# Kernel optimization log

Hardware: AMD Instinct MI355X
Metric: run time of the kernel (lower is better)

The kernel has to match this reference:

```python
import jax, jax.numpy as jnp
import numpy as np

# sarModule stage: in=256, out=512, blocks=2, stride=2, patch_groups=4, mask_size=7
B, C_IN, H, W = 32, 256, 56, 56
C_OUT = 512
PLANES = C_OUT // 4   # Bottleneck inner width = planes // expansion = 128
G = 4                 # patch_groups
MS = 7                # mask_size
TEMP = 1.0            # gumbel-softmax temperature


def conv(x, w, stride=1, pad=0, groups=1):
    return jax.lax.conv_general_dilated(
        x, w, (stride, stride), [(pad, pad), (pad, pad)],
        feature_group_count=groups,
        dimension_numbers=('NCHW', 'OIHW', 'NCHW'))


def bn(x, g, b):
    # BatchNorm in inference form with running_mean=0, running_var=1 folded in
    return x * g[None, :, None, None] + b[None, :, None, None]


def avgpool3s2(x):
    # nn.AvgPool2d(3, stride=2, padding=1), count_include_pad=True
    s = jax.lax.reduce_window(x, 0.0, jax.lax.add, (1, 1, 3, 3), (1, 1, 2, 2),
                              [(0, 0), (0, 0), (1, 1), (1, 1)])
    return s / 9.0


def setup_inputs() -> dict:
    key = jax.random.key(0)
    ks = iter(jax.random.split(key, 64))

    def w(shape):
        fan_in = int(np.prod(shape[1:]))
        return jax.random.normal(next(ks), shape, jnp.float32) * np.float32((2.0 / fan_in) ** 0.5)

    ones = lambda n: jnp.ones((n,), jnp.float32)
    zeros = lambda n: jnp.zeros((n,), jnp.float32)

    x = jax.random.normal(next(ks), (B, C_IN, H, W), jnp.float32)
    u = jax.random.uniform(next(ks), (B, 2, G, MS, MS), jnp.float32, 1e-6, 1.0 - 1e-6)
    gumbel_noise = -jnp.log(-jnp.log(u))

    return dict(
        x=x, gumbel_noise=gumbel_noise,
        # base Bottleneck (256->512, stride 2, downsample = avgpool + 1x1 conv + bn)
        b_w1=w((PLANES, C_IN, 1, 1)), b_g1=ones(PLANES), b_b1=zeros(PLANES),
        b_w2=w((PLANES, PLANES, 3, 3)), b_g2=ones(PLANES), b_b2=zeros(PLANES),
        b_w3=w((C_OUT, PLANES, 1, 1)), b_g3=ones(C_OUT), b_b3=zeros(C_OUT),
        b_dw=w((C_OUT, C_IN, 1, 1)), b_dg=ones(C_OUT), b_db=zeros(C_OUT),
        # refine Bottleneck (256->512, stride 1, downsample = 1x1 conv + bn)
        r_w1=w((PLANES, C_IN, 1, 1)), r_g1=ones(PLANES), r_b1=zeros(PLANES),
        r_w2=w((PLANES, PLANES, 3, 3)), r_g2=ones(PLANES), r_b2=zeros(PLANES),
        r_w3=w((C_OUT, PLANES, 1, 1)), r_g3=ones(C_OUT), r_b3=zeros(C_OUT),
        r_dw=w((C_OUT, C_IN, 1, 1)), r_dg=ones(C_OUT), r_db=zeros(C_OUT),
        # maskGen: grouped 3x3 conv (512 -> 4*G), bn, pool, grouped 1x1 fc (4*G -> 2*G)
        m_w=w((4 * G, C_OUT // G, 3, 3)), m_g=ones(4 * G), m_b=zeros(4 * G),
        m_fcw=w((2 * G, 4, 1, 1)),
        m_fcb=jnp.concatenate([0.1 * ones(G), 5.0 * ones(G)]),  # bias init from maskGen
        # fusion Bottleneck (512->512, stride 2, downsample = avgpool only)
        f_w1=w((PLANES, C_OUT, 1, 1)), f_g1=ones(PLANES), f_b1=zeros(PLANES),
        f_w2=w((PLANES, PLANES, 3, 3)), f_g2=ones(PLANES), f_b2=zeros(PLANES),
        f_w3=w((C_OUT, PLANES, 1, 1)), f_g3=ones(C_OUT), f_b3=zeros(C_OUT),
    )


def reference(x, gumbel_noise,
              b_w1, b_g1, b_b1, b_w2, b_g2, b_b2, b_w3, b_g3, b_b3, b_dw, b_dg, b_db,
              r_w1, r_g1, r_b1, r_w2, r_g2, r_b2, r_w3, r_g3, r_b3, r_dw, r_dg, r_db,
              m_w, m_g, m_b, m_fcw, m_fcb,
              f_w1, f_g1, f_b1, f_w2, f_g2, f_b2, f_w3, f_g3, f_b3):
    # ---- base branch: Bottleneck stride 2, last_relu=False -> [B,512,28,28]
    o = jax.nn.relu(bn(conv(x, b_w1), b_g1, b_b1))
    o = jax.nn.relu(bn(conv(o, b_w2, stride=2, pad=1), b_g2, b_b2))
    o = bn(conv(o, b_w3), b_g3, b_b3)
    x_base = o + bn(conv(avgpool3s2(x), b_dw), b_dg, b_db)

    # ---- maskGen on x_base
    gmap = jax.nn.relu(bn(conv(x_base, m_w, pad=1, groups=G), m_g, m_b))      # [B,16,28,28]
    hb = x_base.shape[2] // MS                                                 # adaptive avgpool 28->7
    gmap = gmap.reshape(B, 4 * G, MS, hb, MS, hb).mean(axis=(3, 5))            # [B,16,7,7]
    logits = conv(gmap, m_fcw, groups=G) + m_fcb[None, :, None, None]          # [B,8,7,7]
    logits = logits.reshape(B, 2, G, MS, MS)                                   # view(B,2,groups,ms,ms)
    # hard gumbel-softmax over dim 1 with straight-through estimator
    y = jax.nn.softmax((logits + gumbel_noise) / TEMP, axis=1)
    hard = jax.nn.one_hot(jnp.argmax(y, axis=1), 2, axis=1, dtype=y.dtype)
    gates = hard + y - jax.lax.stop_gradient(y)
    mask = gates[:, 1]                                                         # [B,G,7,7]

    # nearest-upsample mask x8 and expand across each channel group
    mask_up = jnp.repeat(jnp.repeat(mask, H // MS, axis=-2), W // MS, axis=-1) # [B,G,56,56]
    mask_full = jnp.broadcast_to(mask_up[:, :, None], (B, G, C_OUT // G, H, W)).reshape(B, C_OUT, H, W)

    # ---- refine branch: Bottleneck stride 1, output gated by mask, last_relu=False
    o = jax.nn.relu(bn(conv(x, r_w1), r_g1, r_b1))
    o = jax.nn.relu(bn(conv(o, r_w2, pad=1), r_g2, r_b2))
    o = bn(conv(o, r_w3), r_g3, r_b3) * mask_full
    x_refine = o + bn(conv(x, r_dw), r_dg, r_db)                               # [B,512,56,56]

    # ---- fuse: bilinear upsample base to refine resolution (align_corners=False)
    x_base_up = jax.image.resize(x_base, (B, C_OUT, H, W), 'bilinear')
    fused = jax.nn.relu(x_base_up + x_refine)

    # ---- fusion Bottleneck: stride 2, downsample = avgpool only, last_relu=True
    o = jax.nn.relu(bn(conv(fused, f_w1), f_g1, f_b1))
    o = jax.nn.relu(bn(conv(o, f_w2, stride=2, pad=1), f_g2, f_b2))
    o = bn(conv(o, f_w3), f_g3, f_b3)
    out = jax.nn.relu(o + avgpool3s2(fused))                                   # [B,512,28,28]
    return out, mask
```

## Files before the change

### kernel.cpp

```cpp
#include <hip/hip_runtime.h>
#include <cstdint>

#define BB   32
#define CINX 256
#define HH   56
#define WW   56
#define HWX  3136
#define CO   512
#define PL   128
#define HP   28
#define WP   28
#define HWP  784
#define NG   4
#define MSZ  7

typedef unsigned short ushortT;
typedef unsigned int   uint32;
typedef __attribute__((ext_vector_type(8))) short short8;
typedef __attribute__((ext_vector_type(4))) float f32x4;

__device__ __forceinline__ ushortT f2bf(float f){
  uint32 u = __float_as_uint(f);
  u = (u + 0x7fffu + ((u >> 16) & 1u)) >> 16;
  return (ushortT)u;
}
__device__ __forceinline__ float bf2f(ushortT u){
  return __uint_as_float(((uint32)u) << 16);
}
__device__ __forceinline__ void split2(float v, ushortT& h, ushortT& lo){
  h = f2bf(v);
  lo = f2bf(v - bf2f(h));
}
__device__ __forceinline__ uint32 packu(ushortT a, ushortT b){
  return (uint32)a | ((uint32)b << 16);
}

typedef __attribute__((address_space(1))) const void g_void;
typedef __attribute__((address_space(3))) void l_void;
__device__ __forceinline__ void glds16(const ushortT* g, ushortT* l){
  __builtin_amdgcn_global_load_lds((g_void*)g, (l_void*)l, 16, 0, 0);
}
__device__ __forceinline__ void waitcnt_vm8(){ asm volatile("s_waitcnt vmcnt(8)" ::: "memory"); }
__device__ __forceinline__ void waitcnt_vm0(){ asm volatile("s_waitcnt vmcnt(0)" ::: "memory"); }

__device__ __forceinline__ void wsplit(float v, ushortT* dh, ushortT* dl, size_t i){
  ushortT h, lo; split2(v, h, lo); dh[i] = h; dl[i] = lo;
}

__global__ __launch_bounds__(256) void prep_w(
  const float* __restrict__ b_w1, const float* __restrict__ b_g1,
  const float* __restrict__ b_w2, const float* __restrict__ b_g2,
  const float* __restrict__ b_w3, const float* __restrict__ b_g3,
  const float* __restrict__ b_dw, const float* __restrict__ b_dg,
  const float* __restrict__ r_w1, const float* __restrict__ r_g1,
  const float* __restrict__ r_w2, const float* __restrict__ r_g2,
  const float* __restrict__ r_w3, const float* __restrict__ r_g3,
  const float* __restrict__ r_dw, const float* __restrict__ r_dg,
  const float* __restrict__ f_w1, const float* __restrict__ f_g1,
  const float* __restrict__ f_w2, const float* __restrict__ f_g2,
  const float* __restrict__ f_w3, const float* __restrict__ f_g3,
  const float* __restrict__ b_b1, const float* __restrict__ r_b1,
  ushortT* __restrict__ dh, ushortT* __restrict__ dl,
  ushortT* __restrict__ zp, float* __restrict__ biasC)
{
  const int idx = blockIdx.x*256 + threadIdx.x;
  switch (blockIdx.y){
    case 0: {
      if (idx >= 32768) return; int m = idx >> 8;
      wsplit(b_w1[idx]*b_g1[m], dh, dl, (size_t)0 + idx); } break;
    case 3: {
      if (idx >= 32768) return; int m = idx >> 8;
      wsplit(r_w1[idx]*r_g1[m], dh, dl, 32768 + (size_t)idx); } break;
    case 1: {
      if (idx >= 147456) return; int m = idx / 1152; int k = idx - m*1152;
      int tap = k >> 7, c = k & 127;
      wsplit(b_w2[((size_t)(m*128 + c))*9 + tap]*b_g2[m], dh, dl, 65536 + (size_t)idx); } break;
    case 2: {
      if (idx >= 196608) return; int m = idx / 384; int k = idx - m*384;
      float v = (k < 128) ? b_w3[m*128 + k]*b_g3[m] : b_dw[m*256 + (k-128)]*b_dg[m];
      wsplit(v, dh, dl, 212992 + (size_t)idx); } break;
    case 4: {
      if (idx >= 147456) return; int m = idx / 1152; int k = idx - m*1152;
      int tap = k >> 7, c = k & 127;
      wsplit(r_w2[((size_t)(m*128 + c))*9 + tap]*r_g2[m], dh, dl, 409600 + (size_t)idx); } break;
    case 5: {
      if (idx >= 196608) return; int m = idx / 384; int k = idx - m*384;
      float v = (k < 128) ? r_w3[m*128 + k]*r_g3[m] : r_dw[m*256 + (k-128)]*r_dg[m];
      wsplit(v, dh, dl, 557056 + (size_t)idx); } break;
    case 6: {
      if (idx >= 65536) return; int m = idx >> 9;
      wsplit(f_w1[idx]*f_g1[m], dh, dl, 753664 + (size_t)idx); } break;
    case 7: {
      if (idx >= 147456) return; int m = idx / 1152; int k = idx - m*1152;
      int tap = k >> 7, c = k & 127;
      wsplit(f_w2[((size_t)(m*128 + c))*9 + tap]*f_g2[m], dh, dl, 819200 + (size_t)idx); } break;
    case 8: {
      if (idx >= 65536) return; int m = idx >> 7;
      wsplit(f_w3[idx]*f_g3[m], dh, dl, 966656 + (size_t)idx); } break;
    case 9: {
      if (idx < 64) zp[idx] = 0;
      if (idx < 128) biasC[idx] = b_b1[idx];
      else if (idx < 256) biasC[idx] = r_b1[idx-128];
    } break;
  }
}

__global__ __launch_bounds__(256) void k_pool2(const float* __restrict__ x,
    ushortT* __restrict__ ph_, ushortT* __restrict__ pl_){
  __shared__ float s[16][17];
  const int p0 = blockIdx.x*16, c0 = blockIdx.y*16, bz = blockIdx.z;
  const int ci = threadIdx.x >> 4, pi = threadIdx.x & 15;
  {
    const int p = p0 + pi;
    const int oy = p / WP, ox = p - oy*WP;
    const float* src = x + ((size_t)bz*CINX + c0 + ci)*HWX;
    float sum = 0.f;
    #pragma unroll
    for (int dy=0; dy<3; dy++){
      int yy = 2*oy-1+dy;
      if ((unsigned)yy >= HH) continue;
      #pragma unroll
      for (int dx=0; dx<3; dx++){
        int xx = 2*ox-1+dx;
        if ((unsigned)xx >= WW) continue;
        sum += src[yy*WW + xx];
      }
    }
    s[ci][pi] = sum * (1.f/9.f);
  }
  __syncthreads();
  const int pr = threadIdx.x >> 4, cj = threadIdx.x & 15;
  float v = s[cj][pr];
  ushortT h, lo; split2(v, h, lo);
  size_t o = ((size_t)bz*HWP + p0 + pr)*CINX + c0 + cj;
  ph_[o] = h; pl_[o] = lo;
}

__global__ __launch_bounds__(256) void prep_x2(const float* __restrict__ x,
    ushortT* __restrict__ xh, ushortT* __restrict__ xl){
  __shared__ float s[16][17];
  const int p0 = blockIdx.x*16, c0 = blockIdx.y*16, bz = blockIdx.z;
  const int ci = threadIdx.x >> 4, pi = threadIdx.x & 15;
  s[ci][pi] = x[((size_t)bz*CINX + c0 + ci)*HWX + p0 + pi];
  __syncthreads();
  const int pr = threadIdx.x >> 4, cj = threadIdx.x & 15;
  float v = s[cj][pr];
  ushortT h, lo; split2(v, h, lo);
  size_t o = ((size_t)bz*HWX + p0 + pr)*CINX + c0 + cj;
  xh[o] = h; xl[o] = lo;
}

__global__ __launch_bounds__(256) void k_poolf(const ushortT* __restrict__ fzh,
    const ushortT* __restrict__ fzl, float* __restrict__ pf){
  const int p = blockIdx.x, bz = blockIdx.y;
  const int oy = p / WP, ox = p - oy*WP;
  const int c = threadIdx.x*2;
  float s0 = 0.f, s1 = 0.f;
  #pragma unroll
  for (int dy=0; dy<3; dy++){
    const int iy = 2*oy - 1 + dy;
    if ((unsigned)iy >= (unsigned)HH) continue;
    #pragma unroll
    for (int dx=0; dx<3; dx++){
      const int ix = 2*ox - 1 + dx;
      if ((unsigned)ix >= (unsigned)WW) continue;
      const size_t fi = ((size_t)bz*HWX + (size_t)(iy*WW + ix))*CO + c;
      uint32 hh = *(const uint32*)(fzh + fi);
      uint32 ll = *(const uint32*)(fzl + fi);
      s0 += bf2f((ushortT)(hh & 0xffff)) + bf2f((ushortT)(ll & 0xffff));
      s1 += bf2f((ushortT)(hh >> 16))    + bf2f((ushortT)(ll >> 16));
    }
  }
  const size_t o = ((size_t)bz*HWP + p)*CO + c;
  pf[o]   = s0 * (1.f/9.f);
  pf[o+1] = s1 * (1.f/9.f);
}

template<int KIND,int EPI,int S1F,int MT,int DBUF,int SWAP,int GX,int GY,int STRIDE,int PAD,
         int HIN,int WIN,int WOUT,int NOUT,int C1,int C2,int BSTR1,int MTOT,int KTOT>
__global__ __launch_bounds__(MT*2)
void gemm_bf3(const ushortT* __restrict__ wph, const ushortT* __restrict__ wpl,
              const ushortT* __restrict__ s1h, const ushortT* __restrict__ s1l,
              const ushortT* __restrict__ s2h, const ushortT* __restrict__ s2l,
              const float* __restrict__ xf32,
              const float* __restrict__ bias1, const float* __restrict__ bias2,
              const float* __restrict__ maskf, const float* __restrict__ xbase,
              const ushortT* __restrict__ zp,
              ushortT* __restrict__ oh, ushortT* __restrict__ ol,
              float* __restrict__ of32)
{
  constexpr int NW = MT/32;
  constexpr int BCALLS = 8/NW;
  constexpr bool GATHER1 = (KIND==0 && S1F==1);
  constexpr int BUFSZ = MT*64 + 8192;
  constexpr int T = GX*GY*BB;
  static_assert(T % 8 == 0, "grid not divisible by 8 XCDs");
  constexpr int QX = T/8;
  __shared__ ushortT smem[BUFSZ*(DBUF+1)];

  const int tid = threadIdx.x;
  const int lin = blockIdx.x;
  const int virt = (lin & 7)*QX + (lin >> 3);
  const int vx = virt % GX;
  const int vrest = virt / GX;
  const int vy = vrest % GY;
  const int bz = vrest / GY;
  const int nt = SWAP ? vy : vx;
  const int mt = SWAP ? vx : vy;
  const int l  = tid & 63, w = tid >> 6;
  const int wm = w >> 1, wn = w & 1;

  size_t a_src[2]; int a_dst[2];
  #pragma unroll
  for (int c=0;c<2;c++){
    int s = (w*2 + c)*64 + l;
    int row = s >> 2, slotm = s & 3;
    int logical = slotm ^ ((row >> 1) & 3);
    a_src[c] = (size_t)(mt*MT + row)*KTOT + logical*8;
    a_dst[c] = (w*2 + c)*512;
  }

  int b_dst[2]; size_t b_base1[2], b_base2[2]; int b_klane[2];
  int b_oy[2], b_ox[2]; bool b_ok[2]; float b_mv[2];
  #pragma unroll
  for (int c=0;c<BCALLS;c++){
    int s = (w*BCALLS + c)*64 + l;
    int row = s >> 2, slotm = s & 3;
    int logical = slotm ^ ((row >> 1) & 3);
    b_klane[c] = logical*8;
    b_dst[c] = (w*BCALLS + c)*512;
    int ngr = nt*128 + row;
    b_ok[c] = (ngr < NOUT);
    int oyv = ngr / WOUT, oxv = ngr - (ngr / WOUT)*WOUT;
    b_oy[c] = oyv; b_ox[c] = oxv;
    b_base1[c] = ((size_t)bz*NOUT + ngr)*BSTR1 + b_klane[c];
    b_base2[c] = ((size_t)bz*NOUT + ngr)*C2 + b_klane[c];
    b_mv[c] = 1.f;
    if (KIND == 3)
      b_mv[c] = b_ok[c] ? maskf[((size_t)(bz*NG + mt)*MSZ + (oyv>>3))*MSZ + (oxv>>3)] : 0.f;
  }

  const int sr = tid >> 1;
  const int hp = tid & 1;
  const int swz = (sr >> 1) & 3;
  const int lws0 = sr*32 + ((2*hp) ^ swz)*8;
  const int lws1 = sr*32 + ((2*hp + 1) ^ swz)*8;
  const int ng = nt*128 + sr;

  f32x4 acc[4][4];
  f32x4 zf = {0.f,0.f,0.f,0.f};
  #pragma unroll
  for (int i=0;i<4;i++)
    #pragma unroll
    for (int j=0;j<4;j++) acc[i][j] = zf;

  auto stagef = [&](int ks, ushortT* AHb, ushortT* ALb, ushortT* BHb, ushortT* BLb){
    const int k0 = ks*32;
    #pragma unroll
    for (int c=0;c<2;c++){
      glds16(wph + a_src[c] + k0, AHb + a_dst[c]);
      glds16(wpl + a_src[c] + k0, ALb + a_dst[c]);
    }
    if constexpr (GATHER1){
      if (tid < 256){
        uint4 b0 = make_uint4(0,0,0,0), b1v = b0, b2v = b0, b3v = b0;
        if (ng < NOUT){
          size_t fbase = ((size_t)bz*C1 + k0 + hp*16)*(size_t)NOUT + ng;
          ushortT h[16], lo[16];
          #pragma unroll
          for (int e=0;e<16;e++){ split2(xf32[fbase + (size_t)e*NOUT], h[e], lo[e]); }
          b0  = make_uint4(packu(h[0],h[1]),  packu(h[2],h[3]),  packu(h[4],h[5]),  packu(h[6],h[7]));
          b1v = make_uint4(packu(h[8],h[9]),  packu(h[10],h[11]),packu(h[12],h[13]),packu(h[14],h[15]));
          b2v = make_uint4(packu(lo[0],lo[1]),packu(lo[2],lo[3]),packu(lo[4],lo[5]),packu(lo[6],lo[7]));
          b3v = make_uint4(packu(lo[8],lo[9]),packu(lo[10],lo[11]),packu(lo[12],lo[13]),packu(lo[14],lo[15]));
        }
        *(uint4*)(BHb + lws0) = b0;  *(uint4*)(BHb + lws1) = b1v;
        *(uint4*)(BLb + lws0) = b2v; *(uint4*)(BLb + lws1) = b3v;
      }
    } else {
      #pragma unroll
      for (int c=0;c<BCALLS;c++){
        const ushortT *sh, *sl;
        if constexpr (KIND == 0){
          bool ok = b_ok[c];
          size_t off = b_base1[c] + k0;
          sh = ok ? s1h + off : zp;  sl = ok ? s1l + off : zp;
        } else if constexpr (KIND == 1){
          const int tap = k0 >> 7;
          const int cb  = (k0 & 127);
          const int dy = tap/3, dx = tap - 3*(tap/3);
          int iy = b_oy[c]*STRIDE + dy - PAD;
          int ix = b_ox[c]*STRIDE + dx - PAD;
          bool ok = b_ok[c] && (unsigned)iy < (unsigned)HIN && (unsigned)ix < (unsigned)WIN;
          size_t off = ((size_t)bz*(HIN*WIN) + (size_t)(iy*WIN + ix))*BSTR1 + cb + b_klane[c];
          sh = ok ? s1h + off : zp;  sl = ok ? s1l + off : zp;
        } else {
          if (k0 < C1){
            bool ok = b_ok[c] && (KIND != 3 || b_mv[c] != 0.f);
            size_t off = b_base1[c] + k0;
            sh = ok ? s1h + off : zp;  sl = ok ? s1l + off : zp;
          } else {
            bool ok = b_ok[c];
            size_t off = b_base2[c] + (k0 - C1);
            sh = ok ? s2h + off : zp;  sl = ok ? s2l + off : zp;
          }
        }
        glds16(sh, BHb + b_dst[c]);
        glds16(sl, BLb + b_dst[c]);
      }
    }
  };

  auto computef = [&](const ushortT* AHb, const ushortT* ALb,
                      const ushortT* BHb, const ushortT* BLb){
    short8 bh[4], bl[4];
    #pragma unroll
    for (int nf=0; nf<4; nf++){
      const int rr = wn*64 + nf*16 + (l & 15);
      const int ph = (l >> 4) ^ ((rr >> 1) & 3);
      bh[nf] = *(const short8*)(BHb + rr*32 + ph*8);
      bl[nf] = *(const short8*)(BLb + rr*32 + ph*8);
    }
    #pragma unroll
    for (int mf=0; mf<4; mf++){
      const int rr = wm*64 + mf*16 + (l & 15);
      const int ph = (l >> 4) ^ ((rr >> 1) & 3);
      short8 ah = *(const short8*)(AHb + rr*32 + ph*8);
      short8 al = *(const short8*)(ALb + rr*32 + ph*8);
      #pragma unroll
      for (int nf=0; nf<4; nf++)
        acc[mf][nf] = __builtin_amdgcn_mfma_f32_16x16x32_bf16(ah, bh[nf], acc[mf][nf], 0,0,0);
      #pragma unroll
      for (int nf=0; nf<4; nf++)
        acc[mf][nf] = __builtin_amdgcn_mfma_f32_16x16x32_bf16(ah, bl[nf], acc[mf][nf], 0,0,0);
      #pragma unroll
      for (int nf=0; nf<4; nf++)
        acc[mf][nf] = __builtin_amdgcn_mfma_f32_16x16x32_bf16(al, bh[nf], acc[mf][nf], 0,0,0);
    }
  };

  const int NK = KTOT / 32;
  if constexpr (DBUF == 0){
    ushortT* AH  = smem;
    ushortT* AL  = smem + MT*32;
    ushortT* BHs = smem + MT*64;
    ushortT* BLs = smem + MT*64 + 4096;
    for (int ks=0; ks<NK; ks++){
      stagef(ks, AH, AL, BHs, BLs);
      __syncthreads();
      computef(AH, AL, BHs, BLs);
      __syncthreads();
    }
  } else {
    stagef(0, smem, smem + MT*32, smem + MT*64, smem + MT*64 + 4096);
    waitcnt_vm0();
    __builtin_amdgcn_s_barrier();
    for (int ks=0; ks<NK; ks++){
      ushortT* cb = smem + (ks & 1)*BUFSZ;
      ushortT* nb = smem + ((ks & 1) ^ 1)*BUFSZ;
      if (ks + 1 < NK){
        stagef(ks + 1, nb, nb + MT*32, nb + MT*64, nb + MT*64 + 4096);
        waitcnt_vm8();
      } else {
        waitcnt_vm0();
      }
      __builtin_amdgcn_sched_barrier(0);
      __builtin_amdgcn_s_barrier();
      computef(cb, cb + MT*32, cb + MT*64, cb + MT*64 + 4096);
      __builtin_amdgcn_s_barrier();
    }
  }

  const int mb0 = mt*MT + wm*64;
  const int nb0 = nt*128 + wn*64;

  #pragma unroll
  for (int nf=0; nf<4; nf++){
    const int n = nb0 + nf*16 + (l & 15);
    if (n >= NOUT) continue;
    if constexpr (EPI == 0){
      const size_t ob = ((size_t)bz*NOUT + n)*MTOT;
      #pragma unroll
      for (int mf=0; mf<4; mf++){
        const int m0 = mb0 + mf*16 + (l>>4)*4;
        ushort4 hq, lq; ushortT h0, l0; float v;
        v = fmaxf(acc[mf][nf][0] + bias1[m0+0], 0.f); split2(v,h0,l0); hq.x=h0; lq.x=l0;
        v = fmaxf(acc[mf][nf][1] + bias1[m0+1], 0.f); split2(v,h0,l0); hq.y=h0; lq.y=l0;
        v = fmaxf(acc[mf][nf][2] + bias1[m0+2], 0.f); split2(v,h0,l0); hq.z=h0; lq.z=l0;
        v = fmaxf(acc[mf][nf][3] + bias1[m0+3], 0.f); split2(v,h0,l0); hq.w=h0; lq.w=l0;
        *(ushort4*)(oh + ob + m0) = hq;
        *(ushort4*)(ol + ob + m0) = lq;
      }
    } else if constexpr (EPI == 1){
      #pragma unroll
      for (int mf=0; mf<4; mf++){
        const int m0 = mb0 + mf*16 + (l>>4)*4;
        #pragma unroll
        for (int r=0;r<4;r++){
          const int m = m0 + r;
          of32[((size_t)bz*MTOT + m)*NOUT + n] = acc[mf][nf][r] + bias1[m] + bias2[m];
        }
      }
    } else if constexpr (EPI == 2){
      const int y = n / WOUT, x = n - (n / WOUT)*WOUT;
      const int grpw = (mt*MT + wm*64) >> 7;
      const float mvv = maskf[((size_t)(bz*NG + grpw)*MSZ + (y>>3))*MSZ + (x>>3)];
      const int iy = y >> 1, ix = x >> 1;
      int yA,yB,xA,xB; float wyA,wyB,wxA,wxB;
      if (y & 1){ yA=iy; wyA=0.75f; yB=(iy+1<HP)?iy+1:HP-1; wyB=0.25f; }
      else      { yA=(iy>0)?iy-1:0; wyA=0.25f; yB=iy; wyB=0.75f; }
      if (x & 1){ xA=ix; wxA=0.75f; xB=(ix+1<WP)?ix+1:WP-1; wxB=0.25f; }
      else      { xA=(ix>0)?ix-1:0; wxA=0.25f; xB=ix; wxB=0.75f; }
      const size_t ob = ((size_t)bz*NOUT + n)*MTOT;
      #pragma unroll
      for (int mf=0; mf<4; mf++){
        const int m0 = mb0 + mf*16 + (l>>4)*4;
        ushort4 hq, lq;
        #pragma unroll
        for (int r=0;r<4;r++){
          const int m = m0 + r;
          const float* xb = xbase + ((size_t)bz*MTOT + m)*HWP;
          float up = wyA*(wxA*xb[yA*WP+xA] + wxB*xb[yA*WP+xB])
                   + wyB*(wxA*xb[yB*WP+xA] + wxB*xb[yB*WP+xB]);
          float v = fmaxf(acc[mf][nf][r] + up + mvv*bias1[m] + bias2[m], 0.f);
          ushortT h0, l0; split2(v, h0, l0);
          if      (r==0){hq.x=h0;lq.x=l0;}
          else if (r==1){hq.y=h0;lq.y=l0;}
          else if (r==2){hq.z=h0;lq.z=l0;}
          else          {hq.w=h0;lq.w=l0;}
        }
        *(ushort4*)(oh + ob + m0) = hq;
        *(ushort4*)(ol + ob + m0) = lq;
      }
    } else {
      const float* pfrow = xbase + ((size_t)bz*NOUT + n)*MTOT;
      #pragma unroll
      for (int mf=0; mf<4; mf++){
        const int m0 = mb0 + mf*16 + (l>>4)*4;
        const float4 pv = *(const float4*)(pfrow + m0);
        of32[((size_t)bz*MTOT + m0+0)*NOUT + n] = fmaxf(acc[mf][nf][0] + bias1[m0+0] + pv.x, 0.f);
        of32[((size_t)bz*MTOT + m0+1)*NOUT + n] = fmaxf(acc[mf][nf][1] + bias1[m0+1] + pv.y, 0.f);
        of32[((size_t)bz*MTOT + m0+2)*NOUT + n] = fmaxf(acc[mf][nf][2] + bias1[m0+2] + pv.z, 0.f);
        of32[((size_t)bz*MTOT + m0+3)*NOUT + n] = fmaxf(acc[mf][nf][3] + bias1[m0+3] + pv.w, 0.f);
      }
    }
  }
}

#define GM_LDSW 9216
__global__ __launch_bounds__(256) void k_gmap2(const float* __restrict__ xbase,
    const float* __restrict__ mw, const float* __restrict__ mg, const float* __restrict__ mb,
    float* __restrict__ gmap){
  __shared__ float wsh[GM_LDSW];
  __shared__ float red[16][2][4][16];
  const int tile = blockIdx.x, b = blockIdx.y;
  const int tid = threadIdx.x;
  const int pl = tid & 15, cs = tid >> 4;
  const int p = tile*16 + pl;
  const int oy = p / WP, ox = p - oy*WP;
  int toff[9];
  #pragma unroll
  for (int tap=0; tap<9; tap++){
    int dy = tap/3, dx = tap - 3*dy;
    int yy = oy + dy - 1, xx = ox + dx - 1;
    toff[tap] = ((unsigned)yy < (unsigned)HP && (unsigned)xx < (unsigned)WP) ? (yy*WP + xx) : -1;
  }
  float acc[2][4] = {{0.f,0.f,0.f,0.f},{0.f,0.f,0.f,0.f}};
  for (int pass=0; pass<2; pass++){
    __syncthreads();
    for (int i = tid; i < GM_LDSW; i += 256){
      int ocl = i & 3, tap = (i >> 2) % 9, c_rel = i / 36;
      int cg = pass*256 + c_rel;
      int g = cg >> 7;
      int oc = g*4 + ocl;
      wsh[i] = mw[((size_t)(oc*128 + (cg & 127)))*9 + tap] * mg[oc];
    }
    __syncthreads();
    const float* xb = xbase + ((size_t)b*CO + pass*256 + cs*16)*HWP;
    for (int cl=0; cl<16; cl++){
      const float* xc = xb + (size_t)cl*HWP;
      const float* wr = &wsh[(cs*16 + cl)*36];
      #pragma unroll
      for (int tap=0; tap<9; tap++){
        if (toff[tap] < 0) continue;
        float v = xc[toff[tap]];
        f32x4 w4 = *(const f32x4*)(wr + tap*4);
        acc[pass][0] += v*w4[0];
        acc[pass][1] += v*w4[1];
        acc[pass][2] += v*w4[2];
        acc[pass][3] += v*w4[3];
      }
    }
  }
  #pragma unroll
  for (int pp=0; pp<2; pp++)
    #pragma unroll
    for (int o=0; o<4; o++)
      red[cs][pp][o][pl] = acc[pp][o];
  __syncthreads();
  const int oc = tid >> 4;
  const int g = oc >> 2, ocl = oc & 3, pg = g >> 1, cs0 = (g & 1)*8;
  float s = 0.f;
  #pragma unroll
  for (int t=0; t<8; t++) s += red[cs0 + t][pg][ocl][pl];
  s = fmaxf(s + mb[oc], 0.f);
  gmap[((size_t)b*16 + oc)*HWP + p] = s;
}

__global__ __launch_bounds__(256) void k_gpool(const float* __restrict__ gmap, float* __restrict__ gpool){
  int idx = blockIdx.x*256 + threadIdx.x;
  if (idx >= BB*16*49) return;
  int q = idx % 49; int t = idx / 49; int ch = t % 16; int b = t / 16;
  int my = q/7, mx = q%7;
  const float* src = gmap + ((size_t)b*16 + ch)*HWP;
  float s = 0.f;
  #pragma unroll
  for (int yb=0;yb<4;yb++)
    #pragma unroll
    for (int xb=0;xb<4;xb++)
      s += src[(my*4+yb)*WP + (mx*4+xb)];
  gpool[idx] = s * (1.f/16.f);
}

__global__ __launch_bounds__(256) void k_mask(const float* __restrict__ gpool, const float* __restrict__ fcw,
    const float* __restrict__ fcb, const float* __restrict__ gum,
    float* __restrict__ maskf, float* __restrict__ mout){
// ... 28 lines not shown
  const float* b_w2 = (const float*)d_in[5];
  const float* b_g2 = (const float*)d_in[6];
  const float* b_b2 = (const float*)d_in[7];
  const float* b_w3 = (const float*)d_in[8];
  const float* b_g3 = (const float*)d_in[9];
  const float* b_b3 = (const float*)d_in[10];
  const float* b_dw = (const float*)d_in[11];
  const float* b_dg = (const float*)d_in[12];
  const float* b_db = (const float*)d_in[13];
  const float* r_w1 = (const float*)d_in[14];
  const float* r_g1 = (const float*)d_in[15];
  const float* r_b1 = (const float*)d_in[16];
  const float* r_w2 = (const float*)d_in[17];
  const float* r_g2 = (const float*)d_in[18];
  const float* r_b2 = (const float*)d_in[19];
  const float* r_w3 = (const float*)d_in[20];
  const float* r_g3 = (const float*)d_in[21];
  const float* r_b3 = (const float*)d_in[22];
  const float* r_dw = (const float*)d_in[23];
  const float* r_dg = (const float*)d_in[24];
  const float* r_db = (const float*)d_in[25];
  const float* m_w  = (const float*)d_in[26];
  const float* m_g  = (const float*)d_in[27];
  const float* m_b  = (const float*)d_in[28];
  const float* m_fcw= (const float*)d_in[29];
  const float* m_fcb= (const float*)d_in[30];
  const float* f_w1 = (const float*)d_in[31];
  const float* f_g1 = (const float*)d_in[32];
  const float* f_b1 = (const float*)d_in[33];
  const float* f_w2 = (const float*)d_in[34];
  const float* f_g2 = (const float*)d_in[35];
  const float* f_b2 = (const float*)d_in[36];
  const float* f_w3 = (const float*)d_in[37];
  const float* f_g3 = (const float*)d_in[38];
  const float* f_b3 = (const float*)d_in[39];

  char* ws = (char*)d_ws;
  constexpr size_t O_WPH  = 0;
  constexpr size_t O_WPL  = 2064384;
  constexpr size_t O_CH   = 4128768;
  constexpr size_t O_DH   = 55508992;
  constexpr size_t O_DL   = 61931520;
  constexpr size_t O_EH   = 68354048;
  constexpr size_t O_EL   = 94044160;
  constexpr size_t O_PF   = O_EH;
  constexpr size_t O_XB   = 119734272;
  constexpr size_t O_GMAP = 171114496;
  constexpr size_t O_GPOOL= 172720128;
  constexpr size_t O_MASK = 172820480;
  constexpr size_t O_FH   = 172845568;
  constexpr size_t O_PH   = 172845568;
  constexpr size_t O_PL   = 185690624;
  constexpr size_t O_FL   = 275606016;
  constexpr size_t O_ZP   = 378366464;
  constexpr size_t O_BIASC= 378366592;

  ushortT* WPH = (ushortT*)(ws + O_WPH);
  ushortT* WPL = (ushortT*)(ws + O_WPL);
  ushortT* MGH = (ushortT*)(ws + O_CH);
  ushortT* XH  = (ushortT*)(ws + O_CH);
  ushortT* F1H = (ushortT*)(ws + O_CH);
  ushortT* F1L = (ushortT*)(ws + O_CH + 25690112);
  ushortT* DHp = (ushortT*)(ws + O_DH);
  ushortT* DLp = (ushortT*)(ws + O_DL);
  ushortT* EHp = (ushortT*)(ws + O_EH);
  ushortT* ELp = (ushortT*)(ws + O_EL);
  float*   PF  = (float*)(ws + O_PF);
  float*   XB  = (float*)(ws + O_XB);
  ushortT* PHp = (ushortT*)(ws + O_PH);
  ushortT* PLp = (ushortT*)(ws + O_PL);
  ushortT* FHp = (ushortT*)(ws + O_FH);
  ushortT* FLp = (ushortT*)(ws + O_FL);
  float*   GMAP = (float*)(ws + O_GMAP);
  float*   GPOOL= (float*)(ws + O_GPOOL);
  float*   MASKF= (float*)(ws + O_MASK);
  ushortT* ZP  = (ushortT*)(ws + O_ZP);
  float*   BIASC = (float*)(ws + O_BIASC);
  (void)ws_size;

  float* outp = (float*)d_out;
  float* mout = outp + (size_t)BB*CO*HWP;
  ushortT* dout_u = (ushortT*)d_out;

  dim3 blk(256), blk2(512);
  const ushortT* nu = nullptr; const float* nf_ = nullptr;
  ushortT* nuo = nullptr; float* nfo = nullptr;

  prep_w<<<dim3(768, 10), blk, 0, stream>>>(b_w1,b_g1,b_w2,b_g2,b_w3,b_g3,b_dw,b_dg,
      r_w1,r_g1,r_w2,r_g2,r_w3,r_g3,r_dw,r_dg,f_w1,f_g1,f_w2,f_g2,f_w3,f_g3,
      b_b1, r_b1, WPH, WPL, ZP, BIASC);
  k_pool2<<<dim3(49, 16, BB), blk, 0, stream>>>(x, PHp, PLp);

  gemm_bf3<0,0,1,256,0,0, 25,1, 1,0,56,56,56,3136, 256,0,256, 256,256><<<dim3(800), blk2, 0, stream>>>(
      WPH+0, WPL+0, nu, nu, nu, nu, x, BIASC, nf_, nf_, nf_, ZP, MGH, dout_u, nfo);
  gemm_bf3<1,0,0,128,1,0, 7,1, 2,1,56,56,28,784, 128,0,256, 128,1152><<<dim3(224), blk, 0, stream>>>(
      WPH+65536, WPL+65536, MGH, dout_u, nu, nu, nf_, b_b2, nf_, nf_, nf_, ZP, DHp, DLp, nfo);
  gemm_bf3<2,1,0,256,0,0, 7,2, 1,0,28,28,28,784, 128,256,128, 512,384><<<dim3(448), blk2, 0, stream>>>(
      WPH+212992, WPL+212992, DHp, DLp, PHp, PLp, nf_, b_b3, b_db, nf_, nf_, ZP, nuo, nuo, XB);

  k_gmap2<<<dim3(49, BB), blk, 0, stream>>>(XB, m_w, m_g, m_b, GMAP);
  k_gpool<<<dim3(98), blk, 0, stream>>>(GMAP, GPOOL);
  k_mask<<<dim3(25), blk, 0, stream>>>(GPOOL, m_fcw, m_fcb, gum, MASKF, mout);

  gemm_bf3<1,0,0,128,1,0, 25,1, 1,1,56,56,56,3136, 128,0,256, 128,1152><<<dim3(800), blk, 0, stream>>>(
      WPH+409600, WPL+409600, MGH+128, dout_u+128, nu, nu, nf_, r_b2, nf_, nf_, nf_, ZP, EHp, ELp, nfo);

  prep_x2<<<dim3(196, 16, BB), blk, 0, stream>>>(x, XH, dout_u);

  gemm_bf3<3,2,0,128,1,1, 4,25, 1,0,56,56,56,3136, 128,256,128, 512,384><<<dim3(3200), blk, 0, stream>>>(
      WPH+557056, WPL+557056, EHp, ELp, XH, dout_u, nf_, r_b3, r_db, MASKF, XB, ZP, FHp, FLp, nfo);

  k_poolf<<<dim3(HWP, BB), blk, 0, stream>>>(FHp, FLp, PF);

  gemm_bf3<0,0,0,128,1,0, 25,1, 1,0,56,56,56,3136, 512,0,512, 128,512><<<dim3(800), blk, 0, stream>>>(
      WPH+753664, WPL+753664, FHp, FLp, nu, nu, nf_, f_b1, nf_, nf_, nf_, ZP, F1H, F1L, nfo);
  gemm_bf3<1,0,0,128,1,0, 7,1, 2,1,56,56,28,784, 128,0,128, 128,1152><<<dim3(224), blk, 0, stream>>>(
      WPH+819200, WPL+819200, F1H, F1L, nu, nu, nf_, f_b2, nf_, nf_, nf_, ZP, DHp, DLp, nfo);
  gemm_bf3<0,3,0,256,0,0, 7,2, 1,0,28,28,28,784, 128,0,128, 512,128><<<dim3(448), blk2, 0, stream>>>(
      WPH+966656, WPL+966656, DHp, DLp, nu, nu, nf_, f_b3, nf_, nf_, PF, ZP, nuo, nuo, outp);
}
```

Measured before the change: 1.054 ms.

## Stage GEMM epilogue output through LDS for coalesced stores; vectorize avg-pool kernel

For the bf16-split output epilogues (EPI 0 and 2), the high and low halves of each tile are written to shared memory one after the other. Each thread then writes a contiguous 64-element row segment to global memory with 16-byte stores, replacing scattered 8-byte stores. The pool kernel now handles 8 channels per thread and 4 output pixels per block, using 16-byte loads and float4 stores. The change adds extra barriers, LDS round-trips and register pressure (the low halves are held across the first store phase), and may raise shared memory use for kernels without double buffering.

```diff
diff --git a/kernel.cpp b/kernel.cpp
--- a/kernel.cpp
+++ b/kernel.cpp
@@ -152,10 +152,13 @@
 
 __global__ __launch_bounds__(256) void k_poolf(const ushortT* __restrict__ fzh,
     const ushortT* __restrict__ fzl, float* __restrict__ pf){
-  const int p = blockIdx.x, bz = blockIdx.y;
+  const int pb = blockIdx.x, bz = blockIdx.y;
+  const int psub = threadIdx.x >> 6;
+  const int lane = threadIdx.x & 63;
+  const int p = pb*4 + psub;
   const int oy = p / WP, ox = p - oy*WP;
-  const int c = threadIdx.x*2;
-  float s0 = 0.f, s1 = 0.f;
+  const int c = lane*8;
+  float s[8] = {0.f,0.f,0.f,0.f,0.f,0.f,0.f,0.f};
   #pragma unroll
   for (int dy=0; dy<3; dy++){
     const int iy = 2*oy - 1 + dy;
@@ -165,15 +168,19 @@
       const int ix = 2*ox - 1 + dx;
       if ((unsigned)ix >= (unsigned)WW) continue;
       const size_t fi = ((size_t)bz*HWX + (size_t)(iy*WW + ix))*CO + c;
-      uint32 hh = *(const uint32*)(fzh + fi);
-      uint32 ll = *(const uint32*)(fzl + fi);
-      s0 += bf2f((ushortT)(hh & 0xffff)) + bf2f((ushortT)(ll & 0xffff));
-      s1 += bf2f((ushortT)(hh >> 16))    + bf2f((ushortT)(ll >> 16));
+      uint4 hh = *(const uint4*)(fzh + fi);
+      uint4 ll = *(const uint4*)(fzl + fi);
+      ushortT hv[8], lv[8];
+      *(uint4*)hv = hh; *(uint4*)lv = ll;
+      #pragma unroll
+      for (int j=0;j<8;j++) s[j] += bf2f(hv[j]) + bf2f(lv[j]);
     }
   }
   const size_t o = ((size_t)bz*HWP + p)*CO + c;
-  pf[o]   = s0 * (1.f/9.f);
-  pf[o+1] = s1 * (1.f/9.f);
+  float4 o0 = make_float4(s[0]*(1.f/9.f), s[1]*(1.f/9.f), s[2]*(1.f/9.f), s[3]*(1.f/9.f));
+  float4 o1 = make_float4(s[4]*(1.f/9.f), s[5]*(1.f/9.f), s[6]*(1.f/9.f), s[7]*(1.f/9.f));
+  *(float4*)(pf + o)     = o0;
+  *(float4*)(pf + o + 4) = o1;
 }
 
 template<int KIND,int EPI,int S1F,int MT,int DBUF,int SWAP,int GX,int GY,int STRIDE,int PAD,
@@ -193,10 +200,14 @@
   constexpr int BCALLS = 8/NW;
   constexpr bool GATHER1 = (KIND==0 && S1F==1);
   constexpr int BUFSZ = MT*64 + 8192;
+  constexpr int SSTR = MT + 8;
+  constexpr int STORE_USH = (EPI==0 || EPI==2) ? 128*SSTR : 0;
+  constexpr int STAGE_USH = BUFSZ*(DBUF+1);
+  constexpr int SMEM_USH = (STAGE_USH > STORE_USH) ? STAGE_USH : STORE_USH;
   constexpr int T = GX*GY*BB;
   static_assert(T % 8 == 0, "grid not divisible by 8 XCDs");
   constexpr int QX = T/8;
-  __shared__ ushortT smem[BUFSZ*(DBUF+1)];
+  __shared__ ushortT smem[SMEM_USH];
 
   const int tid = threadIdx.x;
   const int lin = blockIdx.x;
@@ -374,74 +385,122 @@
   const int mb0 = mt*MT + wm*64;
   const int nb0 = nt*128 + wn*64;
 
-  #pragma unroll
-  for (int nf=0; nf<4; nf++){
-    const int n = nb0 + nf*16 + (l & 15);
-    if (n >= NOUT) continue;
-    if constexpr (EPI == 0){
-      const size_t ob = ((size_t)bz*NOUT + n)*MTOT;
+  if constexpr (EPI == 0 || EPI == 2){
+    __syncthreads();
+    ushortT* SP = smem;
+    ushort4 loq[4][4];
+    #pragma unroll
+    for (int nf=0; nf<4; nf++){
+      const int n = nb0 + nf*16 + (l & 15);
+      const int nrel = wn*64 + nf*16 + (l & 15);
+      const bool nok = (n < NOUT);
+      float mvv=0.f, wyA=0.f, wyB=0.f, wxA=0.f, wxB=0.f;
+      int yA=0, yB=0, xA=0, xB=0;
+      if constexpr (EPI == 2){
+        if (nok){
+          const int y = n / WOUT, x = n - (n / WOUT)*WOUT;
+          const int grpw = (mt*MT + wm*64) >> 7;
+          mvv = maskf[((size_t)(bz*NG + grpw)*MSZ + (y>>3))*MSZ + (x>>3)];
+          const int iy = y >> 1, ix = x >> 1;
+          if (y & 1){ yA=iy; wyA=0.75f; yB=(iy+1<HP)?iy+1:HP-1; wyB=0.25f; }
+          else      { yA=(iy>0)?iy-1:0; wyA=0.25f; yB=iy; wyB=0.75f; }
+          if (x & 1){ xA=ix; wxA=0.75f; xB=(ix+1<WP)?ix+1:WP-1; wxB=0.25f; }
+          else      { xA=(ix>0)?ix-1:0; wxA=0.25f; xB=ix; wxB=0.75f; }
+        }
+      }
       #pragma unroll
       for (int mf=0; mf<4; mf++){
         const int m0 = mb0 + mf*16 + (l>>4)*4;
-        ushort4 hq, lq; ushortT h0, l0; float v;
-        v = fmaxf(acc[mf][nf][0] + bias1[m0+0], 0.f); split2(v,h0,l0); hq.x=h0; lq.x=l0;
-        v = fmaxf(acc[mf][nf][1] + bias1[m0+1], 0.f); split2(v,h0,l0); hq.y=h0; lq.y=l0;
-        v = fmaxf(acc[mf][nf][2] + bias1[m0+2], 0.f); split2(v,h0,l0); hq.z=h0; lq.z=l0;
-        v = fmaxf(acc[mf][nf][3] + bias1[m0+3], 0.f); split2(v,h0,l0); hq.w=h0; lq.w=l0;
-        *(ushort4*)(oh + ob + m0) = hq;
-        *(ushort4*)(ol + ob + m0) = lq;
-      }
-    } else if constexpr (EPI == 1){
+        const int mrel = wm*64 + mf*16 + (l>>4)*4;
+        ushort4 hq = make_ushort4(0,0,0,0), lq = make_ushort4(0,0,0,0);
+        if (nok){
+          #pragma unroll
+          for (int r=0;r<4;r++){
+            const int m = m0 + r;
+            float v;
+            if constexpr (EPI == 0){
+              v = fmaxf(acc[mf][nf][r] + bias1[m], 0.f);
+            } else {
+              const float* xb = xbase + ((size_t)bz*MTOT + m)*HWP;
+              float up = wyA*(wxA*xb[yA*WP+xA] + wxB*xb[yA*WP+xB])
+                       + wyB*(wxA*xb[yB*WP+xA] + wxB*xb[yB*WP+xB]);
+              v = fmaxf(acc[mf][nf][r] + up + mvv*bias1[m] + bias2[m], 0.f);
+            }
+            ushortT h0, l0; split2(v, h0, l0);
+            if      (r==0){hq.x=h0;lq.x=l0;}
+            else if (r==1){hq.y=h0;lq.y=l0;}
+            else if (r==2){hq.z=h0;lq.z=l0;}
+            else          {hq.w=h0;lq.w=l0;}
+          }
+        }
+        *(ushort4*)(SP + nrel*SSTR + mrel) = hq;
+        loq[nf][mf] = lq;
+      }
+    }
+    __syncthreads();
+    constexpr int SEGS = MT/64;
+    const int srow = tid / SEGS;
+    const int sseg = tid - srow*SEGS;
+    const int gn = nt*128 + srow;
+    {
+      const ushortT* rp = SP + srow*SSTR + sseg*64;
+      uint4 q[8];
+      #pragma unroll
+      for (int i=0;i<8;i++) q[i] = *(const uint4*)(rp + i*8);
+      if (gn < NOUT){
+        ushortT* gp = oh + ((size_t)bz*NOUT + gn)*MTOT + mt*MT + sseg*64;
+        #pragma unroll
+        for (int i=0;i<8;i++) *(uint4*)(gp + i*8) = q[i];
+      }
+    }
+    __syncthreads();
+    #pragma unroll
+    for (int nf=0; nf<4; nf++){
+      const int nrel = wn*64 + nf*16 + (l & 15);
       #pragma unroll
       for (int mf=0; mf<4; mf++){
-        const int m0 = mb0 + mf*16 + (l>>4)*4;
+        const int mrel = wm*64 + mf*16 + (l>>4)*4;
+        *(ushort4*)(SP + nrel*SSTR + mrel) = loq[nf][mf];
+      }
+    }
+    __syncthreads();
+    {
+      const ushortT* rp = SP + srow*SSTR + sseg*64;
+      uint4 q[8];
+      #pragma unroll
+      for (int i=0;i<8;i++) q[i] = *(const uint4*)(rp + i*8);
+      if (gn < NOUT){
+        ushortT* gp = ol + ((size_t)bz*NOUT + gn)*MTOT + mt*MT + sseg*64;
         #pragma unroll
-        for (int r=0;r<4;r++){
-          const int m = m0 + r;
-          of32[((size_t)bz*MTOT + m)*NOUT + n] = acc[mf][nf][r] + bias1[m] + bias2[m];
+        for (int i=0;i<8;i++) *(uint4*)(gp + i*8) = q[i];
+      }
+    }
+  } else {
+    #pragma unroll
+    for (int nf=0; nf<4; nf++){
+      const int n = nb0 + nf*16 + (l & 15);
+      if (n >= NOUT) continue;
+      if constexpr (EPI == 1){
+        #pragma unroll
+        for (int mf=0; mf<4; mf++){
+          const int m0 = mb0 + mf*16 + (l>>4)*4;
+          #pragma unroll
+          for (int r=0;r<4;r++){
+            const int m = m0 + r;
+            of32[((size_t)bz*MTOT + m)*NOUT + n] = acc[mf][nf][r] + bias1[m] + bias2[m];
+          }
         }
-      }
-    } else if constexpr (EPI == 2){
-      const int y = n / WOUT, x = n - (n / WOUT)*WOUT;
-      const int grpw = (mt*MT + wm*64) >> 7;
-      const float mvv = maskf[((size_t)(bz*NG + grpw)*MSZ + (y>>3))*MSZ + (x>>3)];
-      const int iy = y >> 1, ix = x >> 1;
-      int yA,yB,xA,xB; float wyA,wyB,wxA,wxB;
-      if (y & 1){ yA=iy; wyA=0.75f; yB=(iy+1<HP)?iy+1:HP-1; wyB=0.25f; }
-      else      { yA=(iy>0)?iy-1:0; wyA=0.25f; yB=iy; wyB=0.75f; }
-      if (x & 1){ xA=ix; wxA=0.75f; xB=(ix+1<WP)?ix+1:WP-1; wxB=0.25f; }
-      else      { xA=(ix>0)?ix-1:0; wxA=0.25f; xB=ix; wxB=0.75f; }
-      const size_t ob = ((size_t)bz*NOUT + n)*MTOT;
-      #pragma unroll
-      for (int mf=0; mf<4; mf++){
-        const int m0 = mb0 + mf*16 + (l>>4)*4;
-        ushort4 hq, lq;
+      } else {
+        const float* pfrow = xbase + ((size_t)bz*NOUT + n)*MTOT;
         #pragma unroll
-        for (int r=0;r<4;r++){
-          const int m = m0 + r;
-          const float* xb = xbase + ((size_t)bz*MTOT + m)*HWP;
-          float up = wyA*(wxA*xb[yA*WP+xA] + wxB*xb[yA*WP+xB])
-                   + wyB*(wxA*xb[yB*WP+xA] + wxB*xb[yB*WP+xB]);
-          float v = fmaxf(acc[mf][nf][r] + up + mvv*bias1[m] + bias2[m], 0.f);
-          ushortT h0, l0; split2(v, h0, l0);
-          if      (r==0){hq.x=h0;lq.x=l0;}
-          else if (r==1){hq.y=h0;lq.y=l0;}
-          else if (r==2){hq.z=h0;lq.z=l0;}
-          else          {hq.w=h0;lq.w=l0;}
+        for (int mf=0; mf<4; mf++){
+          const int m0 = mb0 + mf*16 + (l>>4)*4;
+          const float4 pv = *(const float4*)(pfrow + m0);
+          of32[((size_t)bz*MTOT + m0+0)*NOUT + n] = fmaxf(acc[mf][nf][0] + bias1[m0+0] + pv.x, 0.f);
+          of32[((size_t)bz*MTOT + m0+1)*NOUT + n] = fmaxf(acc[mf][nf][1] + bias1[m0+1] + pv.y, 0.f);
+          of32[((size_t)bz*MTOT + m0+2)*NOUT + n] = fmaxf(acc[mf][nf][2] + bias1[m0+2] + pv.z, 0.f);
+          of32[((size_t)bz*MTOT + m0+3)*NOUT + n] = fmaxf(acc[mf][nf][3] + bias1[m0+3] + pv.w, 0.f);
         }
-        *(ushort4*)(oh + ob + m0) = hq;
-        *(ushort4*)(ol + ob + m0) = lq;
-      }
-    } else {
-      const float* pfrow = xbase + ((size_t)bz*NOUT + n)*MTOT;
-      #pragma unroll
-      for (int mf=0; mf<4; mf++){
-        const int m0 = mb0 + mf*16 + (l>>4)*4;
-        const float4 pv = *(const float4*)(pfrow + m0);
-        of32[((size_t)bz*MTOT + m0+0)*NOUT + n] = fmaxf(acc[mf][nf][0] + bias1[m0+0] + pv.x, 0.f);
-        of32[((size_t)bz*MTOT + m0+1)*NOUT + n] = fmaxf(acc[mf][nf][1] + bias1[m0+1] + pv.y, 0.f);
-        of32[((size_t)bz*MTOT + m0+2)*NOUT + n] = fmaxf(acc[mf][nf][2] + bias1[m0+2] + pv.z, 0.f);
-        of32[((size_t)bz*MTOT + m0+3)*NOUT + n] = fmaxf(acc[mf][nf][3] + bias1[m0+3] + pv.w, 0.f);
       }
     }
   }
@@ -664,7 +723,7 @@
   gemm_bf3<3,2,0,128,1,1, 4,25, 1,0,56,56,56,3136, 128,256,128, 512,384><<<dim3(3200), blk, 0, stream>>>(
       WPH+557056, WPL+557056, EHp, ELp, XH, dout_u, nf_, r_b3, r_db, MASKF, XB, ZP, FHp, FLp, nfo);
 
-  k_poolf<<<dim3(HWP, BB), blk, 0, stream>>>(FHp, FLp, PF);
+  k_poolf<<<dim3(196, BB), blk, 0, stream>>>(FHp, FLp, PF);
 
   gemm_bf3<0,0,0,128,1,0, 25,1, 1,0,56,56,56,3136, 512,0,512, 128,512><<<dim3(800), blk, 0, stream>>>(
       WPH+753664, WPL+753664, FHp, FLp, nu, nu, nf_, f_b1, nf_, nf_, nf_, ZP, F1H, F1L, nfo);
```

New measurement: 1.085 ms. 1.03x slower.

## Run MT=128 GEMMs with 8 waves per block and vectorize pooling kernel

Applied to the files above, without the earlier changes.

Adds a wave-count template parameter so the MT=128 GEMMs launch 512 threads, laid out as 2x4 waves with two N-fragments each instead of 4 waves with four. This halves the accumulators and LDS loads per wave, which should give more latency hiding and better occupancy. The per-thread A/B staging counts and the vmcnt wait thresholds are adjusted to match. Separately, the fused avgpool kernel now handles four output pixels per block with 16-byte loads and stores. The cost is lower MFMA-per-LDS-read reuse per wave in the GEMMs.

```diff
diff --git a/kernel.cpp b/kernel.cpp
--- a/kernel.cpp
+++ b/kernel.cpp
@@ -40,8 +40,6 @@
 __device__ __forceinline__ void glds16(const ushortT* g, ushortT* l){
   __builtin_amdgcn_global_load_lds((g_void*)g, (l_void*)l, 16, 0, 0);
 }
-__device__ __forceinline__ void waitcnt_vm8(){ asm volatile("s_waitcnt vmcnt(8)" ::: "memory"); }
-__device__ __forceinline__ void waitcnt_vm0(){ asm volatile("s_waitcnt vmcnt(0)" ::: "memory"); }
 
 __device__ __forceinline__ void wsplit(float v, ushortT* dh, ushortT* dl, size_t i){
   ushortT h, lo; split2(v, h, lo); dh[i] = h; dl[i] = lo;
@@ -152,10 +150,13 @@
 
 __global__ __launch_bounds__(256) void k_poolf(const ushortT* __restrict__ fzh,
     const ushortT* __restrict__ fzl, float* __restrict__ pf){
-  const int p = blockIdx.x, bz = blockIdx.y;
+  const int pb = blockIdx.x, bz = blockIdx.y;
+  const int psub = threadIdx.x >> 6;
+  const int lane = threadIdx.x & 63;
+  const int p = pb*4 + psub;
   const int oy = p / WP, ox = p - oy*WP;
-  const int c = threadIdx.x*2;
-  float s0 = 0.f, s1 = 0.f;
+  const int c = lane*8;
+  float s[8] = {0.f,0.f,0.f,0.f,0.f,0.f,0.f,0.f};
   #pragma unroll
   for (int dy=0; dy<3; dy++){
     const int iy = 2*oy - 1 + dy;
@@ -165,20 +166,25 @@
       const int ix = 2*ox - 1 + dx;
       if ((unsigned)ix >= (unsigned)WW) continue;
       const size_t fi = ((size_t)bz*HWX + (size_t)(iy*WW + ix))*CO + c;
-      uint32 hh = *(const uint32*)(fzh + fi);
-      uint32 ll = *(const uint32*)(fzl + fi);
-      s0 += bf2f((ushortT)(hh & 0xffff)) + bf2f((ushortT)(ll & 0xffff));
-      s1 += bf2f((ushortT)(hh >> 16))    + bf2f((ushortT)(ll >> 16));
+      uint4 hh = *(const uint4*)(fzh + fi);
+      uint4 ll = *(const uint4*)(fzl + fi);
+      ushortT hv[8], lv[8];
+      *(uint4*)hv = hh; *(uint4*)lv = ll;
+      #pragma unroll
+      for (int j=0;j<8;j++) s[j] += bf2f(hv[j]) + bf2f(lv[j]);
     }
   }
   const size_t o = ((size_t)bz*HWP + p)*CO + c;
-  pf[o]   = s0 * (1.f/9.f);
-  pf[o+1] = s1 * (1.f/9.f);
-}
-
-template<int KIND,int EPI,int S1F,int MT,int DBUF,int SWAP,int GX,int GY,int STRIDE,int PAD,
-         int HIN,int WIN,int WOUT,int NOUT,int C1,int C2,int BSTR1,int MTOT,int KTOT>
-__global__ __launch_bounds__(MT*2)
+  float4 o0 = make_float4(s[0]*(1.f/9.f), s[1]*(1.f/9.f), s[2]*(1.f/9.f), s[3]*(1.f/9.f));
+  float4 o1 = make_float4(s[4]*(1.f/9.f), s[5]*(1.f/9.f), s[6]*(1.f/9.f), s[7]*(1.f/9.f));
+  *(float4*)(pf + o)     = o0;
+  *(float4*)(pf + o + 4) = o1;
+}
+
+template<int KIND,int EPI,int S1F,int MT,int NWV,int DBUF,int SWAP,int GX,int GY,
+         int STRIDE,int PAD,int HIN,int WIN,int WOUT,int NOUT,int C1,int C2,
+         int BSTR1,int MTOT,int KTOT>
+__global__ __launch_bounds__(NWV*64)
 void gemm_bf3(const ushortT* __restrict__ wph, const ushortT* __restrict__ wpl,
               const ushortT* __restrict__ s1h, const ushortT* __restrict__ s1l,
               const ushortT* __restrict__ s2h, const ushortT* __restrict__ s2l,
@@ -189,10 +195,13 @@
               ushortT* __restrict__ oh, ushortT* __restrict__ ol,
               float* __restrict__ of32)
 {
-  constexpr int NW = MT/32;
-  constexpr int BCALLS = 8/NW;
+  constexpr int ACALLS  = MT/(16*NWV);
+  constexpr int BCALLS2 = 8/NWV;
+  constexpr int GLDS_PER = (ACALLS + BCALLS2)*2;
   constexpr bool GATHER1 = (KIND==0 && S1F==1);
   constexpr int BUFSZ = MT*64 + 8192;
+  constexpr int WNs = (MT==256) ? 2 : (NWV==8 ? 4 : 2);
+  constexpr int NF  = 128/(WNs*16);
   constexpr int T = GX*GY*BB;
   static_assert(T % 8 == 0, "grid not divisible by 8 XCDs");
   constexpr int QX = T/8;
@@ -208,27 +217,27 @@
   const int nt = SWAP ? vy : vx;
   const int mt = SWAP ? vx : vy;
   const int l  = tid & 63, w = tid >> 6;
-  const int wm = w >> 1, wn = w & 1;
+  const int wm = w / WNs, wn = w % WNs;
 
   size_t a_src[2]; int a_dst[2];
   #pragma unroll
-  for (int c=0;c<2;c++){
-    int s = (w*2 + c)*64 + l;
+  for (int c=0;c<ACALLS;c++){
+    int s = (w*ACALLS + c)*64 + l;
     int row = s >> 2, slotm = s & 3;
     int logical = slotm ^ ((row >> 1) & 3);
     a_src[c] = (size_t)(mt*MT + row)*KTOT + logical*8;
-    a_dst[c] = (w*2 + c)*512;
+    a_dst[c] = (w*ACALLS + c)*512;
   }
 
   int b_dst[2]; size_t b_base1[2], b_base2[2]; int b_klane[2];
   int b_oy[2], b_ox[2]; bool b_ok[2]; float b_mv[2];
   #pragma unroll
-  for (int c=0;c<BCALLS;c++){
-    int s = (w*BCALLS + c)*64 + l;
+  for (int c=0;c<BCALLS2;c++){
+    int s = (w*BCALLS2 + c)*64 + l;
     int row = s >> 2, slotm = s & 3;
     int logical = slotm ^ ((row >> 1) & 3);
     b_klane[c] = logical*8;
-    b_dst[c] = (w*BCALLS + c)*512;
+    b_dst[c] = (w*BCALLS2 + c)*512;
     int ngr = nt*128 + row;
     b_ok[c] = (ngr < NOUT);
     int oyv = ngr / WOUT, oxv = ngr - (ngr / WOUT)*WOUT;
@@ -257,7 +266,7 @@
   auto stagef = [&](int ks, ushortT* AHb, ushortT* ALb, ushortT* BHb, ushortT* BLb){
     const int k0 = ks*32;
     #pragma unroll
-    for (int c=0;c<2;c++){
+    for (int c=0;c<ACALLS;c++){
       glds16(wph + a_src[c] + k0, AHb + a_dst[c]);
       glds16(wpl + a_src[c] + k0, ALb + a_dst[c]);
     }
@@ -279,7 +288,7 @@
       }
     } else {
       #pragma unroll
-      for (int c=0;c<BCALLS;c++){
+      for (int c=0;c<BCALLS2;c++){
         const ushortT *sh, *sl;
         if constexpr (KIND == 0){
           bool ok = b_ok[c];
@@ -313,10 +322,10 @@
 
   auto computef = [&](const ushortT* AHb, const ushortT* ALb,
                       const ushortT* BHb, const ushortT* BLb){
-    short8 bh[4], bl[4];
-    #pragma unroll
-    for (int nf=0; nf<4; nf++){
-      const int rr = wn*64 + nf*16 + (l & 15);
+    short8 bh[NF], bl[NF];
+    #pragma unroll
+    for (int nf=0; nf<NF; nf++){
+      const int rr = wn*(NF*16) + nf*16 + (l & 15);
       const int ph = (l >> 4) ^ ((rr >> 1) & 3);
       bh[nf] = *(const short8*)(BHb + rr*32 + ph*8);
       bl[nf] = *(const short8*)(BLb + rr*32 + ph*8);
@@ -328,13 +337,13 @@
       short8 ah = *(const short8*)(AHb + rr*32 + ph*8);
       short8 al = *(const short8*)(ALb + rr*32 + ph*8);
       #pragma unroll
-      for (int nf=0; nf<4; nf++)
+      for (int nf=0; nf<NF; nf++)
         acc[mf][nf] = __builtin_amdgcn_mfma_f32_16x16x32_bf16(ah, bh[nf], acc[mf][nf], 0,0,0);
       #pragma unroll
-      for (int nf=0; nf<4; nf++)
+      for (int nf=0; nf<NF; nf++)
         acc[mf][nf] = __builtin_amdgcn_mfma_f32_16x16x32_bf16(ah, bl[nf], acc[mf][nf], 0,0,0);
       #pragma unroll
-      for (int nf=0; nf<4; nf++)
+      for (int nf=0; nf<NF; nf++)
         acc[mf][nf] = __builtin_amdgcn_mfma_f32_16x16x32_bf16(al, bh[nf], acc[mf][nf], 0,0,0);
     }
   };
@@ -353,16 +362,19 @@
     }
   } else {
     stagef(0, smem, smem + MT*32, smem + MT*64, smem + MT*64 + 4096);
-    waitcnt_vm0();
+    asm volatile("s_waitcnt vmcnt(0)" ::: "memory");
     __builtin_amdgcn_s_barrier();
     for (int ks=0; ks<NK; ks++){
       ushortT* cb = smem + (ks & 1)*BUFSZ;
       ushortT* nb = smem + ((ks & 1) ^ 1)*BUFSZ;
       if (ks + 1 < NK){
         stagef(ks + 1, nb, nb + MT*32, nb + MT*64, nb + MT*64 + 4096);
-        waitcnt_vm8();
+        if constexpr (GLDS_PER == 4)
+          asm volatile("s_waitcnt vmcnt(4)" ::: "memory");
+        else
+          asm volatile("s_waitcnt vmcnt(8)" ::: "memory");
       } else {
-        waitcnt_vm0();
+        asm volatile("s_waitcnt vmcnt(0)" ::: "memory");
       }
       __builtin_amdgcn_sched_barrier(0);
       __builtin_amdgcn_s_barrier();
@@ -372,10 +384,10 @@
   }
 
   const int mb0 = mt*MT + wm*64;
-  const int nb0 = nt*128 + wn*64;
-
-  #pragma unroll
-  for (int nf=0; nf<4; nf++){
+  const int nb0 = nt*128 + wn*(NF*16);
+
+  #pragma unroll
+  for (int nf=0; nf<NF; nf++){
     const int n = nb0 + nf*16 + (l & 15);
     if (n >= NOUT) continue;
     if constexpr (EPI == 0){
@@ -636,7 +648,7 @@
   float* mout = outp + (size_t)BB*CO*HWP;
   ushortT* dout_u = (ushortT*)d_out;
 
-  dim3 blk(256), blk2(512);
+  dim3 blk(256), blk512(512);
   const ushortT* nu = nullptr; const float* nf_ = nullptr;
   ushortT* nuo = nullptr; float* nfo = nullptr;
 
@@ -645,31 +657,31 @@
       b_b1, r_b1, WPH, WPL, ZP, BIASC);
   k_pool2<<<dim3(49, 16, BB), blk, 0, stream>>>(x, PHp, PLp);
 
-  gemm_bf3<0,0,1,256,0,0, 25,1, 1,0,56,56,56,3136, 256,0,256, 256,256><<<dim3(800), blk2, 0, stream>>>(
+  gemm_bf3<0,0,1,256,8,0,0, 25,1, 1,0,56,56,56,3136, 256,0,256, 256,256><<<dim3(800), blk512, 0, stream>>>(
       WPH+0, WPL+0, nu, nu, nu, nu, x, BIASC, nf_, nf_, nf_, ZP, MGH, dout_u, nfo);
-  gemm_bf3<1,0,0,128,1,0, 7,1, 2,1,56,56,28,784, 128,0,256, 128,1152><<<dim3(224), blk, 0, stream>>>(
+  gemm_bf3<1,0,0,128,8,1,0, 7,1, 2,1,56,56,28,784, 128,0,256, 128,1152><<<dim3(224), blk512, 0, stream>>>(
       WPH+65536, WPL+65536, MGH, dout_u, nu, nu, nf_, b_b2, nf_, nf_, nf_, ZP, DHp, DLp, nfo);
-  gemm_bf3<2,1,0,256,0,0, 7,2, 1,0,28,28,28,784, 128,256,128, 512,384><<<dim3(448), blk2, 0, stream>>>(
+  gemm_bf3<2,1,0,256,8,0,0, 7,2, 1,0,28,28,28,784, 128,256,128, 512,384><<<dim3(448), blk512, 0, stream>>>(
       WPH+212992, WPL+212992, DHp, DLp, PHp, PLp, nf_, b_b3, b_db, nf_, nf_, ZP, nuo, nuo, XB);
 
   k_gmap2<<<dim3(49, BB), blk, 0, stream>>>(XB, m_w, m_g, m_b, GMAP);
   k_gpool<<<dim3(98), blk, 0, stream>>>(GMAP, GPOOL);
   k_mask<<<dim3(25), blk, 0, stream>>>(GPOOL, m_fcw, m_fcb, gum, MASKF, mout);
 
-  gemm_bf3<1,0,0,128,1,0, 25,1, 1,1,56,56,56,3136, 128,0,256, 128,1152><<<dim3(800), blk, 0, stream>>>(
+  gemm_bf3<1,0,0,128,8,1,0, 25,1, 1,1,56,56,56,3136, 128,0,256, 128,1152><<<dim3(800), blk512, 0, stream>>>(
       WPH+409600, WPL+409600, MGH+128, dout_u+128, nu, nu, nf_, r_b2, nf_, nf_, nf_, ZP, EHp, ELp, nfo);
 
   prep_x2<<<dim3(196, 16, BB), blk, 0, stream>>>(x, XH, dout_u);
 
-  gemm_bf3<3,2,0,128,1,1, 4,25, 1,0,56,56,56,3136, 128,256,128, 512,384><<<dim3(3200), blk, 0, stream>>>(
+  gemm_bf3<3,2,0,128,8,1,1, 4,25, 1,0,56,56,56,3136, 128,256,128, 512,384><<<dim3(3200), blk512, 0, stream>>>(
       WPH+557056, WPL+557056, EHp, ELp, XH, dout_u, nf_, r_b3, r_db, MASKF, XB, ZP, FHp, FLp, nfo);
 
-  k_poolf<<<dim3(HWP, BB), blk, 0, stream>>>(FHp, FLp, PF);
-
-  gemm_bf3<0,0,0,128,1,0, 25,1, 1,0,56,56,56,3136, 512,0,512, 128,512><<<dim3(800), blk, 0, stream>>>(
+  k_poolf<<<dim3(196, BB), blk, 0, stream>>>(FHp, FLp, PF);
+
+  gemm_bf3<0,0,0,128,8,1,0, 25,1, 1,0,56,56,56,3136, 512,0,512, 128,512><<<dim3(800), blk512, 0, stream>>>(
       WPH+753664, WPL+753664, FHp, FLp, nu, nu, nf_, f_b1, nf_, nf_, nf_, ZP, F1H, F1L, nfo);
-  gemm_bf3<1,0,0,128,1,0, 7,1, 2,1,56,56,28,784, 128,0,128, 128,1152><<<dim3(224), blk, 0, stream>>>(
+  gemm_bf3<1,0,0,128,8,1,0, 7,1, 2,1,56,56,28,784, 128,0,128, 128,1152><<<dim3(224), blk512, 0, stream>>>(
       WPH+819200, WPL+819200, F1H, F1L, nu, nu, nf_, f_b2, nf_, nf_, nf_, ZP, DHp, DLp, nfo);
-  gemm_bf3<0,3,0,256,0,0, 7,2, 1,0,28,28,28,784, 128,0,128, 512,128><<<dim3(448), blk2, 0, stream>>>(
+  gemm_bf3<0,3,0,256,8,0,0, 7,2, 1,0,28,28,28,784, 128,0,128, 512,128><<<dim3(448), blk512, 0, stream>>>(
       WPH+966656, WPL+966656, DHp, DLp, nu, nu, nf_, f_b3, nf_, nf_, PF, ZP, nuo, nuo, outp);
 }
```

Result: no change. 1.051 ms (-0.3%).
